# Kernel tuning notes

Measured on AMD Instinct MI355X. Metric: run time of the kernel, lower is better.

Reference implementation:

```python
import jax, jax.numpy as jnp
from jax import lax
import numpy as np

T, B, D, N = 1024, 32, 1024, 64
INIT_D_ALPHA, INIT_ALPHA_BIAS = 0.1, 2.0

def _xavier(key, n_out, n_in):
    lim = float(np.sqrt(6.0 / (n_in + n_out)))
    return jax.random.uniform(key, (n_out, n_in), jnp.float32, -lim, lim)

def setup_inputs() -> dict:
    key = jax.random.key(0)
    k = jax.random.split(key, 5)
    return {
        "x": jax.random.normal(k[0], (T, B, D), jnp.float32),
        "S0": jnp.zeros((B, N, N), jnp.float32),
        "W_k": _xavier(k[1], N, D),
        "W_v": _xavier(k[2], N, D),
        "W_q": _xavier(k[3], N, D),
        "W_alpha": _xavier(k[4], N, D),
        "d_alpha": jnp.full((N,), INIT_D_ALPHA, jnp.float32),
        "b_alpha": jnp.full((N,), INIT_ALPHA_BIAS, jnp.float32),
    }

def reference(x, S0, W_k, W_v, W_q, W_alpha, d_alpha, b_alpha):
    # Precompute all per-step projections as batched GEMMs: [T,B,N]
    k = jnp.einsum('tbd,nd->tbn', x, W_k)
    v = jnp.einsum('tbd,nd->tbn', x, W_v)
    q = jnp.einsum('tbd,nd->tbn', x, W_q)
    ax = jnp.einsum('tbd,nd->tbn', x, W_alpha)

    def step(S, inp):
        k_t, v_t, q_t, ax_t = inp  # each [B,N]
        retrieved = jnp.einsum('bij,bj->bi', S, k_t)            # S @ k
        alpha = jax.nn.sigmoid(ax_t + d_alpha * retrieved + b_alpha)  # [B,N]
        outer = v_t[:, :, None] * k_t[:, None, :]               # outer(v,k) [B,N,N]
        S = alpha[:, :, None] * S + (1.0 - alpha)[:, :, None] * outer
        h = jnp.einsum('bij,bj->bi', S, q_t)                    # S @ q
        out = h * jax.nn.silu(h)                                # self-gated
        return S, out

    S_final, output = lax.scan(step, S0, (k, v, q, ax))
    return output, S_final
```

## Files before the change

### kernel.cpp

```cpp
#include <hip/hip_runtime.h>
#include <math.h>

#define T_STEPS 1024
#define BATCH   32
#define DIM     1024
#define NST     64
#define TBN     ((size_t)T_STEPS * BATCH * NST)

typedef __attribute__((ext_vector_type(8))) short bf16x8;
typedef __attribute__((ext_vector_type(4))) float f32x4;

#define NLOG2E (-1.44269504088896340736f)

__device__ unsigned short g_khi[TBN];
__device__ unsigned short g_klo[TBN];
__device__ unsigned short g_qhi[TBN];
__device__ unsigned short g_qlo[TBN];

__device__ __forceinline__ void gload16(const void* g, void* l)
{
    __builtin_amdgcn_global_load_lds(
        (const __attribute__((address_space(1))) unsigned int*)g,
        (__attribute__((address_space(3))) unsigned int*)l, 16, 0, 0);
}

__device__ __forceinline__ void cvt8(float4 v0, float4 v1, bf16x8& hi, bf16x8& lo)
{
    float f[8] = {v0.x, v0.y, v0.z, v0.w, v1.x, v1.y, v1.z, v1.w};
    bf16x8 h, l;
    #pragma unroll
    for (int i = 0; i < 8; i++) {
        unsigned b = __float_as_uint(f[i]);
        h[i] = (short)(b >> 16);
        l[i] = (short)(__float_as_uint(f[i] - __uint_as_float(b & 0xffff0000u)) >> 16);
    }
    hi = h; lo = l;
}


__global__ __launch_bounds__(512, 1)
void proj_gemm_v2(const float* __restrict__ x,
                  const float* __restrict__ Wk,
                  const float* __restrict__ Wv,
                  const float* __restrict__ Wq,
                  const float* __restrict__ Wa,
                  const float* __restrict__ b_alpha,
                  float* __restrict__ ws)
{
    __shared__ float As[2][128][32];
    __shared__ float Bs[2][256][32];

    const int tid  = threadIdx.x;
    const int lane = tid & 63;
    const int w    = tid >> 6;
    const int m0   = blockIdx.x * 128;

    const int lrow  = lane >> 3;
    const int lgran = (lane & 7) ^ lrow;
    const float* ap0 = x + (size_t)(m0 + 16*w +     lrow) * DIM + lgran * 4;
    const float* ap1 = x + (size_t)(m0 + 16*w + 8 + lrow) * DIM + lgran * 4;
    const float* Wsrc = (w < 2) ? Wk : (w < 4) ? Wv : (w < 6) ? Wq : Wa;
    const float* bp0 = Wsrc + (size_t)((w & 1)*32 +  0 + lrow) * DIM + lgran * 4;
    const float* bp1 = Wsrc + (size_t)((w & 1)*32 +  8 + lrow) * DIM + lgran * 4;
    const float* bp2 = Wsrc + (size_t)((w & 1)*32 + 16 + lrow) * DIM + lgran * 4;
    const float* bp3 = Wsrc + (size_t)((w & 1)*32 + 24 + lrow) * DIM + lgran * 4;

    auto stage = [&](int kb, int buf) {
        const int ko = kb * 32;
        gload16(ap0 + ko, &As[buf][16*w     ][0]);
        gload16(ap1 + ko, &As[buf][16*w +  8][0]);
        gload16(bp0 + ko, &Bs[buf][32*w     ][0]);
        gload16(bp1 + ko, &Bs[buf][32*w +  8][0]);
        gload16(bp2 + ko, &Bs[buf][32*w + 16][0]);
        gload16(bp3 + ko, &Bs[buf][32*w + 24][0]);
    };

    const int fr = lane & 15;
    const int qi = lane >> 4;
    const int sx = fr & 7;
    const int mh = w >> 2;
    const int nq = w & 3;

    f32x4 acc[4][4];
    #pragma unroll
    for (int i = 0; i < 4; i++)
        #pragma unroll
        for (int j = 0; j < 4; j++)
            acc[i][j] = (f32x4)0.0f;

    stage(0, 0);
    __syncthreads();

    #pragma unroll 1
    for (int kb = 0; kb < 32; kb++) {
        const int buf = kb & 1;
        if (kb + 1 < 32) stage(kb + 1, buf ^ 1);

        bf16x8 ah[4], al[4], bh[4], bl[4];
        #pragma unroll
        for (int mt = 0; mt < 4; mt++) {
            const float* rp = &As[buf][mh*64 + mt*16 + fr][0];
            float4 v0 = *(const float4*)(rp + (((2*qi    ) ^ sx) * 4));
            float4 v1 = *(const float4*)(rp + (((2*qi + 1) ^ sx) * 4));
            cvt8(v0, v1, ah[mt], al[mt]);
        }
        #pragma unroll
        for (int nt = 0; nt < 4; nt++) {
            const float* rp = &Bs[buf][nq*64 + nt*16 + fr][0];
            float4 v0 = *(const float4*)(rp + (((2*qi    ) ^ sx) * 4));
            float4 v1 = *(const float4*)(rp + (((2*qi + 1) ^ sx) * 4));
            cvt8(v0, v1, bh[nt], bl[nt]);
        }
        #pragma unroll
        for (int mt = 0; mt < 4; mt++)
            #pragma unroll
            for (int nt = 0; nt < 4; nt++) {
                acc[mt][nt] = __builtin_amdgcn_mfma_f32_16x16x32_bf16(ah[mt], bh[nt], acc[mt][nt], 0, 0, 0);
                acc[mt][nt] = __builtin_amdgcn_mfma_f32_16x16x32_bf16(al[mt], bh[nt], acc[mt][nt], 0, 0, 0);
                acc[mt][nt] = __builtin_amdgcn_mfma_f32_16x16x32_bf16(ah[mt], bl[nt], acc[mt][nt], 0, 0, 0);
            }

        __syncthreads();
    }

    float* outb = ws + (size_t)nq * TBN;
    const int r0 = qi * 4;
    float bav[4];
    #pragma unroll
    for (int nt = 0; nt < 4; nt++)
        bav[nt] = (nq == 3) ? b_alpha[nt*16 + fr] : 0.0f;
    const float scl = (nq == 3) ? NLOG2E : 1.0f;
    #pragma unroll
    for (int mt = 0; mt < 4; mt++)
        #pragma unroll
        for (int nt = 0; nt < 4; nt++)
            #pragma unroll
            for (int r = 0; r < 4; r++) {
                const float val = (acc[mt][nt][r] + bav[nt]) * scl;
                const size_t idx = (size_t)(m0 + mh*64 + mt*16 + r0 + r) * NST + nt*16 + fr;
                if (nq != 2)
                    outb[idx] = val;
                if (nq == 0 || nq == 2) {
                    const unsigned bits = __float_as_uint(val);
                    const unsigned short hi = (unsigned short)(bits >> 16);
                    const float lof = val - __uint_as_float(bits & 0xffff0000u);
                    const unsigned short lo = (unsigned short)(__float_as_uint(lof) >> 16);
                    if (nq == 0) { g_khi[idx] = hi; g_klo[idx] = lo; }
                    else         { g_qhi[idx] = hi; g_qlo[idx] = lo; }
                }
            }
}


#define SCH 16
#define NCH (T_STEPS / SCH)

__global__ __launch_bounds__(256, 2)
void scan_gram2(const float* __restrict__ ws,
                const float* __restrict__ S0,
                const float* __restrict__ d_alpha,
                float* __restrict__ out)
{
    const float* kb_ = ws;
    const float* vb_ = ws + TBN;
    const float* ab_ = ws + 3 * TBN;

    __shared__ float k_st[2][SCH][64];
    __shared__ float va  [2][SCH][16];
    __shared__ float GG  [2][SCH][16][2];
    __shared__ unsigned short KH[2][SCH][64];
    __shared__ unsigned short KL[2][SCH][64];
    __shared__ unsigned short QH[2][SCH][64];
    __shared__ unsigned short QL[2][SCH][64];
    __shared__ float S_pvt[4][64];

    const int tid  = threadIdx.x;
    const int lane = tid & 63;
    const int w    = tid >> 6;
    const int bid  = blockIdx.x;
    const int b    = (bid & 7) * 4 + ((bid >> 3) & 3);
    const int rg   = bid >> 5;
    const int row  = rg * 4 + w;
    const int fr   = lane & 15;
    const int qi   = lane >> 4;

    const size_t stp = (size_t)BATCH * NST;

    float S = S0[((size_t)b * NST + row) * NST + lane];
    const float da_s = d_alpha[row] * NLOG2E;

    const float* ksrc = kb_ + (size_t)(4*w + qi) * stp + (size_t)b * NST + fr * 4;
    const float* vsrc = ((lane & 1) ? ab_ : vb_)
                      + (size_t)(lane >> 2) * stp + (size_t)b * NST + rg * 4;

    const unsigned short* pl_g = (w == 0) ? g_khi : (w == 1) ? g_klo
                               : (w == 2) ? g_qhi : g_qlo;
    const int prow  = lane >> 3;
    const int pgran = (lane & 7) ^ prow;
    const unsigned short* psrc0 = pl_g + ((size_t)prow       * stp + (size_t)b * NST + pgran * 8);
    const unsigned short* psrc1 = pl_g + ((size_t)(8 + prow) * stp + (size_t)b * NST + pgran * 8);

    auto stage = [&](int ch, int buf) {
        const size_t koff = (size_t)ch * SCH * stp;
        gload16(ksrc + koff, &k_st[buf][4*w][0]);
        if (w == 0)
            gload16(vsrc + koff, &va[buf][0][0]);
        unsigned short* pdst = (w == 0) ? &KH[buf][0][0] : (w == 1) ? &KL[buf][0][0]
                             : (w == 2) ? &QH[buf][0][0] : &QL[buf][0][0];
        gload16(psrc0 + koff, pdst);
        gload16(psrc1 + koff, pdst + 8 * 64);
    };

    const int c1 = (qi ^ (fr & 7)) * 8;
    const int c2 = c1 ^ 32;

    stage(0, 0);
    __syncthreads();

    float* op = out + (size_t)b * NST + row;
    float hv = 0.0f;

    #pragma unroll 1
    for (int ch = 0; ch < NCH; ch++) {
        const int buf = ch & 1;

        const bf16x8 Kh0 = *(const bf16x8*)&KH[buf][fr][c1];
        const bf16x8 Kh1 = *(const bf16x8*)&KH[buf][fr][c2];
        const bf16x8 Kl0 = *(const bf16x8*)&KL[buf][fr][c1];
        const bf16x8 Kl1 = *(const bf16x8*)&KL[buf][fr][c2];
        const bf16x8 Qh0 = *(const bf16x8*)&QH[buf][fr][c1];
        const bf16x8 Qh1 = *(const bf16x8*)&QH[buf][fr][c2];
        const bf16x8 Ql0 = *(const bf16x8*)&QL[buf][fr][c1];
        const bf16x8 Ql1 = *(const bf16x8*)&QL[buf][fr][c2];

        S_pvt[w][lane] = S;
        bf16x8 Sh0, Sl0, Sh1, Sl1;
        {
            float4 s0 = *(const float4*)&S_pvt[w][qi * 8];
            float4 s1 = *(const float4*)&S_pvt[w][qi * 8 + 4];
            cvt8(s0, s1, Sh0, Sl0);
            float4 s2 = *(const float4*)&S_pvt[w][32 + qi * 8];
            float4 s3 = *(const float4*)&S_pvt[w][32 + qi * 8 + 4];
            cvt8(s2, s3, Sh1, Sl1);
        }

        f32x4 aR0 = (f32x4)0.0f, aR1 = (f32x4)0.0f;
        f32x4 aH0 = (f32x4)0.0f, aH1 = (f32x4)0.0f;
        aR0 = __builtin_amdgcn_mfma_f32_16x16x32_bf16(Sh0, Kh0, aR0, 0, 0, 0);
        aR0 = __builtin_amdgcn_mfma_f32_16x16x32_bf16(Sh0, Kl0, aR0, 0, 0, 0);
        aR0 = __builtin_amdgcn_mfma_f32_16x16x32_bf16(Sl0, Kh0, aR0, 0, 0, 0);
        aR1 = __builtin_amdgcn_mfma_f32_16x16x32_bf16(Sh1, Kh1, aR1, 0, 0, 0);
        aR1 = __builtin_amdgcn_mfma_f32_16x16x32_bf16(Sh1, Kl1, aR1, 0, 0, 0);
        aR1 = __builtin_amdgcn_mfma_f32_16x16x32_bf16(Sl1, Kh1, aR1, 0, 0, 0);
        aH0 = __builtin_amdgcn_mfma_f32_16x16x32_bf16(Sh0, Qh0, aH0, 0, 0, 0);
        aH0 = __builtin_amdgcn_mfma_f32_16x16x32_bf16(Sh0, Ql0, aH0, 0, 0, 0);
        aH0 = __builtin_amdgcn_mfma_f32_16x16x32_bf16(Sl0, Qh0, aH0, 0, 0, 0);
        aH1 = __builtin_amdgcn_mfma_f32_16x16x32_bf16(Sh1, Qh1, aH1, 0, 0, 0);
        aH1 = __builtin_amdgcn_mfma_f32_16x16x32_bf16(Sh1, Ql1, aH1, 0, 0, 0);
        aH1 = __builtin_amdgcn_mfma_f32_16x16x32_bf16(Sl1, Qh1, aH1, 0, 0, 0);
        float R = aR0[0] + aR1[0];
        float H = aH0[0] + aH1[0];

        if (w == 0) {
            f32x4 aG = (f32x4)0.0f;
            aG = __builtin_amdgcn_mfma_f32_16x16x32_bf16(Kh0, Kh0, aG, 0, 0, 0);
            aG = __builtin_amdgcn_mfma_f32_16x16x32_bf16(Kh0, Kl0, aG, 0, 0, 0);
            aG = __builtin_amdgcn_mfma_f32_16x16x32_bf16(Kl0, Kh0, aG, 0, 0, 0);
            aG = __builtin_amdgcn_mfma_f32_16x16x32_bf16(Kh1, Kh1, aG, 0, 0, 0);
            aG = __builtin_amdgcn_mfma_f32_16x16x32_bf16(Kh1, Kl1, aG, 0, 0, 0);
            aG = __builtin_amdgcn_mfma_f32_16x16x32_bf16(Kl1, Kh1, aG, 0, 0, 0);
            #pragma unroll
            for (int r = 0; r < 4; r++) GG[buf][qi*4 + r][fr][0] = aG[r];
        } else if (w == 1) {
            f32x4 aQ = (f32x4)0.0f;
            aQ = __builtin_amdgcn_mfma_f32_16x16x32_bf16(Kh0, Qh0, aQ, 0, 0, 0);
            aQ = __builtin_amdgcn_mfma_f32_16x16x32_bf16(Kh0, Ql0, aQ, 0, 0, 0);
            aQ = __builtin_amdgcn_mfma_f32_16x16x32_bf16(Kl0, Qh0, aQ, 0, 0, 0);
            aQ = __builtin_amdgcn_mfma_f32_16x16x32_bf16(Kh1, Qh1, aQ, 0, 0, 0);
            aQ = __builtin_amdgcn_mfma_f32_16x16x32_bf16(Kh1, Ql1, aQ, 0, 0, 0);
            aQ = __builtin_amdgcn_mfma_f32_16x16x32_bf16(Kl1, Qh1, aQ, 0, 0, 0);
            #pragma unroll
            for (int r = 0; r < 4; r++) GG[buf][qi*4 + r][fr][1] = aQ[r];
        }

        __syncthreads();

        if (ch + 1 < NCH) stage(ch + 1, buf ^ 1);

        #pragma unroll
        for (int s = 0; s < SCH; s++) {
            const float  kcv = k_st[buf][s][lane];
            const float2 g2  = *(const float2*)&GG[buf][s][fr][0];
            const float  vv  = va[buf][s][w];
            const float  aa  = va[buf][s][4 + w];

            const float ret   = __int_as_float(
                __builtin_amdgcn_readlane(__float_as_int(R), s));
            const float z     = fmaf(da_s, ret, aa);
            const float e     = __builtin_amdgcn_exp2f(z);
            const float alpha = __builtin_amdgcn_rcpf(1.0f + e);
            const float bt    = (1.0f - alpha) * vv;

            R = fmaf(alpha, R, bt * g2.x);
            H = fmaf(alpha, H, bt * g2.y);
            S = fmaf(alpha, S, bt * kcv);

            hv = (lane == s) ? H : hv;
        }

        {
            const float sg = __builtin_amdgcn_rcpf(1.0f + __builtin_amdgcn_exp2f(hv * NLOG2E));
            const float o  = hv * hv * sg;
            if (lane < SCH)
                op[(size_t)(ch * SCH + lane) * stp] = o;
        }

        __syncthreads();
    }

    out[TBN + ((size_t)b * NST + row) * NST + lane] = S;
}


extern "C" void kernel_launch(void* const* d_in, const int* in_sizes, int n_in,
                              void* d_out, int out_size, void* d_ws, size_t ws_size,
                              hipStream_t stream)
{
    const float* x  = (const float*)d_in[0];
    const float* S0 = (const float*)d_in[1];
    const float* Wk = (const float*)d_in[2];
    const float* Wv = (const float*)d_in[3];
    const float* Wq = (const float*)d_in[4];
    const float* Wa = (const float*)d_in[5];
    const float* da = (const float*)d_in[6];
    const float* ba = (const float*)d_in[7];
    float* out = (float*)d_out;
    float* ws  = (float*)d_ws;

    proj_gemm_v2<<<dim3((T_STEPS * BATCH) / 128), 512, 0, stream>>>(x, Wk, Wv, Wq, Wa, ba, ws);

    scan_gram2<<<dim3(BATCH * 16), 256, 0, stream>>>(ws, S0, da, out);
}
```

Measured before the change: 382.2 us.

## Split projection GEMM across column halves and pipeline gram/retrieval in scan

The projection GEMM now runs two 256-thread blocks per 128-row tile, each covering two of the four projections, which doubles the grid and allows two blocks per CU. The scan kernel moves to triple-buffered staging and computes the K·K and K·Q gram for the next chunk ahead of time, so one barrier per chunk is removed. The inner recurrence is software-pipelined so the retrieved value for step s+1 comes from the previous R and gram value rather than waiting on the current update, shortening the serial dependency chain. The cost is more LDS, reloading x twice in the GEMM, and more complex register state in the scan loop.

```diff
diff --git a/kernel.cpp b/kernel.cpp
--- a/kernel.cpp
+++ b/kernel.cpp
@@ -11,6 +11,7 @@
 typedef __attribute__((ext_vector_type(4))) float f32x4;
 
 #define NLOG2E (-1.44269504088896340736f)
+#define MFMA16(a, b, c) __builtin_amdgcn_mfma_f32_16x16x32_bf16(a, b, c, 0, 0, 0)
 
 __device__ unsigned short g_khi[TBN];
 __device__ unsigned short g_klo[TBN];
@@ -38,8 +39,8 @@
 }
 
 
-__global__ __launch_bounds__(512, 1)
-void proj_gemm_v2(const float* __restrict__ x,
+__global__ __launch_bounds__(256, 2)
+void proj_gemm_v3(const float* __restrict__ x,
                   const float* __restrict__ Wk,
                   const float* __restrict__ Wv,
                   const float* __restrict__ Wq,
@@ -48,38 +49,41 @@
                   float* __restrict__ ws)
 {
     __shared__ float As[2][128][32];
-    __shared__ float Bs[2][256][32];
+    __shared__ float Bs[2][128][32];
 
     const int tid  = threadIdx.x;
     const int lane = tid & 63;
     const int w    = tid >> 6;
-    const int m0   = blockIdx.x * 128;
+    const int m0   = (blockIdx.x >> 1) * 128;
+    const int nh   = blockIdx.x & 1;
 
     const int lrow  = lane >> 3;
     const int lgran = (lane & 7) ^ lrow;
-    const float* ap0 = x + (size_t)(m0 + 16*w +     lrow) * DIM + lgran * 4;
-    const float* ap1 = x + (size_t)(m0 + 16*w + 8 + lrow) * DIM + lgran * 4;
-    const float* Wsrc = (w < 2) ? Wk : (w < 4) ? Wv : (w < 6) ? Wq : Wa;
-    const float* bp0 = Wsrc + (size_t)((w & 1)*32 +  0 + lrow) * DIM + lgran * 4;
-    const float* bp1 = Wsrc + (size_t)((w & 1)*32 +  8 + lrow) * DIM + lgran * 4;
-    const float* bp2 = Wsrc + (size_t)((w & 1)*32 + 16 + lrow) * DIM + lgran * 4;
-    const float* bp3 = Wsrc + (size_t)((w & 1)*32 + 24 + lrow) * DIM + lgran * 4;
+    const float* ap[4];
+    #pragma unroll
+    for (int i = 0; i < 4; i++)
+        ap[i] = x + (size_t)(m0 + 32*w + 8*i + lrow) * DIM + lgran * 4;
+    const int proj = nh * 2 + (w >> 1);
+    const float* Wsrc = (proj == 0) ? Wk : (proj == 1) ? Wv : (proj == 2) ? Wq : Wa;
+    const float* bp[4];
+    #pragma unroll
+    for (int i = 0; i < 4; i++)
+        bp[i] = Wsrc + (size_t)((w & 1)*32 + 8*i + lrow) * DIM + lgran * 4;
 
     auto stage = [&](int kb, int buf) {
         const int ko = kb * 32;
-        gload16(ap0 + ko, &As[buf][16*w     ][0]);
-        gload16(ap1 + ko, &As[buf][16*w +  8][0]);
-        gload16(bp0 + ko, &Bs[buf][32*w     ][0]);
-        gload16(bp1 + ko, &Bs[buf][32*w +  8][0]);
-        gload16(bp2 + ko, &Bs[buf][32*w + 16][0]);
-        gload16(bp3 + ko, &Bs[buf][32*w + 24][0]);
+        #pragma unroll
+        for (int i = 0; i < 4; i++) {
+            gload16(ap[i] + ko, &As[buf][32*w + 8*i][0]);
+            gload16(bp[i] + ko, &Bs[buf][32*w + 8*i][0]);
+        }
     };
 
     const int fr = lane & 15;
     const int qi = lane >> 4;
     const int sx = fr & 7;
-    const int mh = w >> 2;
-    const int nq = w & 3;
+    const int mh  = w >> 1;
+    const int nqh = w & 1;
 
     f32x4 acc[4][4];
     #pragma unroll
@@ -106,7 +110,7 @@
         }
         #pragma unroll
         for (int nt = 0; nt < 4; nt++) {
-            const float* rp = &Bs[buf][nq*64 + nt*16 + fr][0];
+            const float* rp = &Bs[buf][nqh*64 + nt*16 + fr][0];
             float4 v0 = *(const float4*)(rp + (((2*qi    ) ^ sx) * 4));
             float4 v1 = *(const float4*)(rp + (((2*qi + 1) ^ sx) * 4));
             cvt8(v0, v1, bh[nt], bl[nt]);
@@ -115,14 +119,15 @@
         for (int mt = 0; mt < 4; mt++)
             #pragma unroll
             for (int nt = 0; nt < 4; nt++) {
-                acc[mt][nt] = __builtin_amdgcn_mfma_f32_16x16x32_bf16(ah[mt], bh[nt], acc[mt][nt], 0, 0, 0);
-                acc[mt][nt] = __builtin_amdgcn_mfma_f32_16x16x32_bf16(al[mt], bh[nt], acc[mt][nt], 0, 0, 0);
-                acc[mt][nt] = __builtin_amdgcn_mfma_f32_16x16x32_bf16(ah[mt], bl[nt], acc[mt][nt], 0, 0, 0);
+                acc[mt][nt] = MFMA16(ah[mt], bh[nt], acc[mt][nt]);
+                acc[mt][nt] = MFMA16(al[mt], bh[nt], acc[mt][nt]);
+                acc[mt][nt] = MFMA16(ah[mt], bl[nt], acc[mt][nt]);
             }
 
         __syncthreads();
     }
 
+    const int nq = nh * 2 + nqh;
     float* outb = ws + (size_t)nq * TBN;
     const int r0 = qi * 4;
     float bav[4];
@@ -156,7 +161,7 @@
 #define NCH (T_STEPS / SCH)
 
 __global__ __launch_bounds__(256, 2)
-void scan_gram2(const float* __restrict__ ws,
+void scan_gram3(const float* __restrict__ ws,
                 const float* __restrict__ S0,
                 const float* __restrict__ d_alpha,
                 float* __restrict__ out)
@@ -165,13 +170,13 @@
     const float* vb_ = ws + TBN;
     const float* ab_ = ws + 3 * TBN;
 
-    __shared__ float k_st[2][SCH][64];
-    __shared__ float va  [2][SCH][16];
+    __shared__ float k_st[3][SCH][64];
+    __shared__ float va  [3][SCH][16];
     __shared__ float GG  [2][SCH][16][2];
-    __shared__ unsigned short KH[2][SCH][64];
-    __shared__ unsigned short KL[2][SCH][64];
-    __shared__ unsigned short QH[2][SCH][64];
-    __shared__ unsigned short QL[2][SCH][64];
+    __shared__ unsigned short KH[3][SCH][64];
+    __shared__ unsigned short KL[3][SCH][64];
+    __shared__ unsigned short QH[3][SCH][64];
+    __shared__ unsigned short QL[3][SCH][64];
     __shared__ float S_pvt[4][64];
 
     const int tid  = threadIdx.x;
@@ -214,24 +219,55 @@
     const int c1 = (qi ^ (fr & 7)) * 8;
     const int c2 = c1 ^ 32;
 
+    auto gram = [&](int fbs, int gdst) {
+        if (w == 0) {
+            const bf16x8 kh0 = *(const bf16x8*)&KH[fbs][fr][c1];
+            const bf16x8 kh1 = *(const bf16x8*)&KH[fbs][fr][c2];
+            const bf16x8 kl0 = *(const bf16x8*)&KL[fbs][fr][c1];
+            const bf16x8 kl1 = *(const bf16x8*)&KL[fbs][fr][c2];
+            f32x4 aG = (f32x4)0.0f;
+            aG = MFMA16(kh0, kh0, aG); aG = MFMA16(kh0, kl0, aG); aG = MFMA16(kl0, kh0, aG);
+            aG = MFMA16(kh1, kh1, aG); aG = MFMA16(kh1, kl1, aG); aG = MFMA16(kl1, kh1, aG);
+            #pragma unroll
+            for (int r = 0; r < 4; r++) GG[gdst][qi*4 + r][fr][0] = aG[r];
+        } else if (w == 1) {
+            const bf16x8 kh0 = *(const bf16x8*)&KH[fbs][fr][c1];
+            const bf16x8 kh1 = *(const bf16x8*)&KH[fbs][fr][c2];
+            const bf16x8 kl0 = *(const bf16x8*)&KL[fbs][fr][c1];
+            const bf16x8 kl1 = *(const bf16x8*)&KL[fbs][fr][c2];
+            const bf16x8 qh0 = *(const bf16x8*)&QH[fbs][fr][c1];
+            const bf16x8 qh1 = *(const bf16x8*)&QH[fbs][fr][c2];
+            const bf16x8 ql0 = *(const bf16x8*)&QL[fbs][fr][c1];
+            const bf16x8 ql1 = *(const bf16x8*)&QL[fbs][fr][c2];
+            f32x4 aQ = (f32x4)0.0f;
+            aQ = MFMA16(kh0, qh0, aQ); aQ = MFMA16(kh0, ql0, aQ); aQ = MFMA16(kl0, qh0, aQ);
+            aQ = MFMA16(kh1, qh1, aQ); aQ = MFMA16(kh1, ql1, aQ); aQ = MFMA16(kl1, qh1, aQ);
+            #pragma unroll
+            for (int r = 0; r < 4; r++) GG[gdst][qi*4 + r][fr][1] = aQ[r];
+        }
+    };
+
     stage(0, 0);
+    stage(1, 1);
     __syncthreads();
+    gram(0, 0);
+    __syncthreads();
 
     float* op = out + (size_t)b * NST + row;
-    float hv = 0.0f;
 
     #pragma unroll 1
     for (int ch = 0; ch < NCH; ch++) {
-        const int buf = ch & 1;
-
-        const bf16x8 Kh0 = *(const bf16x8*)&KH[buf][fr][c1];
-        const bf16x8 Kh1 = *(const bf16x8*)&KH[buf][fr][c2];
-        const bf16x8 Kl0 = *(const bf16x8*)&KL[buf][fr][c1];
-        const bf16x8 Kl1 = *(const bf16x8*)&KL[buf][fr][c2];
-        const bf16x8 Qh0 = *(const bf16x8*)&QH[buf][fr][c1];
-        const bf16x8 Qh1 = *(const bf16x8*)&QH[buf][fr][c2];
-        const bf16x8 Ql0 = *(const bf16x8*)&QL[buf][fr][c1];
-        const bf16x8 Ql1 = *(const bf16x8*)&QL[buf][fr][c2];
+        const int fb = ch % 3;
+        const int gb = ch & 1;
+
+        const bf16x8 Kh0 = *(const bf16x8*)&KH[fb][fr][c1];
+        const bf16x8 Kh1 = *(const bf16x8*)&KH[fb][fr][c2];
+        const bf16x8 Kl0 = *(const bf16x8*)&KL[fb][fr][c1];
+        const bf16x8 Kl1 = *(const bf16x8*)&KL[fb][fr][c2];
+        const bf16x8 Qh0 = *(const bf16x8*)&QH[fb][fr][c1];
+        const bf16x8 Qh1 = *(const bf16x8*)&QH[fb][fr][c2];
+        const bf16x8 Ql0 = *(const bf16x8*)&QL[fb][fr][c1];
+        const bf16x8 Ql1 = *(const bf16x8*)&QL[fb][fr][c2];
 
         S_pvt[w][lane] = S;
         bf16x8 Sh0, Sl0, Sh1, Sl1;
@@ -246,66 +282,57 @@
 
         f32x4 aR0 = (f32x4)0.0f, aR1 = (f32x4)0.0f;
         f32x4 aH0 = (f32x4)0.0f, aH1 = (f32x4)0.0f;
-        aR0 = __builtin_amdgcn_mfma_f32_16x16x32_bf16(Sh0, Kh0, aR0, 0, 0, 0);
-        aR0 = __builtin_amdgcn_mfma_f32_16x16x32_bf16(Sh0, Kl0, aR0, 0, 0, 0);
-        aR0 = __builtin_amdgcn_mfma_f32_16x16x32_bf16(Sl0, Kh0, aR0, 0, 0, 0);
-        aR1 = __builtin_amdgcn_mfma_f32_16x16x32_bf16(Sh1, Kh1, aR1, 0, 0, 0);
-        aR1 = __builtin_amdgcn_mfma_f32_16x16x32_bf16(Sh1, Kl1, aR1, 0, 0, 0);
-        aR1 = __builtin_amdgcn_mfma_f32_16x16x32_bf16(Sl1, Kh1, aR1, 0, 0, 0);
-        aH0 = __builtin_amdgcn_mfma_f32_16x16x32_bf16(Sh0, Qh0, aH0, 0, 0, 0);
-        aH0 = __builtin_amdgcn_mfma_f32_16x16x32_bf16(Sh0, Ql0, aH0, 0, 0, 0);
-        aH0 = __builtin_amdgcn_mfma_f32_16x16x32_bf16(Sl0, Qh0, aH0, 0, 0, 0);
-        aH1 = __builtin_amdgcn_mfma_f32_16x16x32_bf16(Sh1, Qh1, aH1, 0, 0, 0);
-        aH1 = __builtin_amdgcn_mfma_f32_16x16x32_bf16(Sh1, Ql1, aH1, 0, 0, 0);
-        aH1 = __builtin_amdgcn_mfma_f32_16x16x32_bf16(Sl1, Qh1, aH1, 0, 0, 0);
+        aR0 = MFMA16(Sh0, Kh0, aR0); aR0 = MFMA16(Sh0, Kl0, aR0); aR0 = MFMA16(Sl0, Kh0, aR0);
+        aR1 = MFMA16(Sh1, Kh1, aR1); aR1 = MFMA16(Sh1, Kl1, aR1); aR1 = MFMA16(Sl1, Kh1, aR1);
+        aH0 = MFMA16(Sh0, Qh0, aH0); aH0 = MFMA16(Sh0, Ql0, aH0); aH0 = MFMA16(Sl0, Qh0, aH0);
+        aH1 = MFMA16(Sh1, Qh1, aH1); aH1 = MFMA16(Sh1, Ql1, aH1); aH1 = MFMA16(Sl1, Qh1, aH1);
         float R = aR0[0] + aR1[0];
         float H = aH0[0] + aH1[0];
 
-        if (w == 0) {
-            f32x4 aG = (f32x4)0.0f;
-            aG = __builtin_amdgcn_mfma_f32_16x16x32_bf16(Kh0, Kh0, aG, 0, 0, 0);
-            aG = __builtin_amdgcn_mfma_f32_16x16x32_bf16(Kh0, Kl0, aG, 0, 0, 0);
-            aG = __builtin_amdgcn_mfma_f32_16x16x32_bf16(Kl0, Kh0, aG, 0, 0, 0);
-            aG = __builtin_amdgcn_mfma_f32_16x16x32_bf16(Kh1, Kh1, aG, 0, 0, 0);
-            aG = __builtin_amdgcn_mfma_f32_16x16x32_bf16(Kh1, Kl1, aG, 0, 0, 0);
-            aG = __builtin_amdgcn_mfma_f32_16x16x32_bf16(Kl1, Kh1, aG, 0, 0, 0);
-            #pragma unroll
-            for (int r = 0; r < 4; r++) GG[buf][qi*4 + r][fr][0] = aG[r];
-        } else if (w == 1) {
-            f32x4 aQ = (f32x4)0.0f;
-            aQ = __builtin_amdgcn_mfma_f32_16x16x32_bf16(Kh0, Qh0, aQ, 0, 0, 0);
-            aQ = __builtin_amdgcn_mfma_f32_16x16x32_bf16(Kh0, Ql0, aQ, 0, 0, 0);
-            aQ = __builtin_amdgcn_mfma_f32_16x16x32_bf16(Kl0, Qh0, aQ, 0, 0, 0);
-            aQ = __builtin_amdgcn_mfma_f32_16x16x32_bf16(Kh1, Qh1, aQ, 0, 0, 0);
-            aQ = __builtin_amdgcn_mfma_f32_16x16x32_bf16(Kh1, Ql1, aQ, 0, 0, 0);
-            aQ = __builtin_amdgcn_mfma_f32_16x16x32_bf16(Kl1, Qh1, aQ, 0, 0, 0);
-            #pragma unroll
-            for (int r = 0; r < 4; r++) GG[buf][qi*4 + r][fr][1] = aQ[r];
-        }
-
-        __syncthreads();
-
-        if (ch + 1 < NCH) stage(ch + 1, buf ^ 1);
+        if (ch + 1 < NCH) gram((ch + 1) % 3, gb ^ 1);
+
+        if (ch + 2 < NCH) stage(ch + 2, (ch + 2) % 3);
+
+        float alpha_p = 1.0f, vv_p = 0.0f;
+        float g_p = 0.0f, gq_p = 0.0f, kc_p = 0.0f;
+        float vvG  = 0.0f;
+        float diff = __int_as_float(__builtin_amdgcn_readlane(__float_as_int(R), 0));
+        float hv   = 0.0f;
 
         #pragma unroll
         for (int s = 0; s < SCH; s++) {
-            const float  kcv = k_st[buf][s][lane];
-            const float2 g2  = *(const float2*)&GG[buf][s][fr][0];
-            const float  vv  = va[buf][s][w];
-            const float  aa  = va[buf][s][4 + w];
-
-            const float ret   = __int_as_float(
-                __builtin_amdgcn_readlane(__float_as_int(R), s));
+            const float2 g2  = *(const float2*)&GG[gb][s][fr][0];
+            const float  kcv = k_st[fb][s][lane];
+            const float  vv  = va[fb][s][w];
+            const float  aa  = va[fb][s][4 + w];
+
+            const float bt_p = (1.0f - alpha_p) * vv_p;
+            R = fmaf(alpha_p, R, bt_p * g_p);
+            H = fmaf(alpha_p, H, bt_p * gq_p);
+            S = fmaf(alpha_p, S, bt_p * kc_p);
+            if (s >= 1) hv = (lane == s - 1) ? H : hv;
+
+            const float rlR = __int_as_float(__builtin_amdgcn_readlane(__float_as_int(R), s + 1));
+            const float rlG = __int_as_float(__builtin_amdgcn_readlane(__float_as_int(g2.x), s + 1));
+
+            const float ret   = fmaf(alpha_p, diff, vvG);
             const float z     = fmaf(da_s, ret, aa);
             const float e     = __builtin_amdgcn_exp2f(z);
             const float alpha = __builtin_amdgcn_rcpf(1.0f + e);
-            const float bt    = (1.0f - alpha) * vv;
-
-            R = fmaf(alpha, R, bt * g2.x);
-            H = fmaf(alpha, H, bt * g2.y);
-            S = fmaf(alpha, S, bt * kcv);
-
-            hv = (lane == s) ? H : hv;
+
+            const float vvG_n  = vv * rlG;
+            const float diff_n = rlR - vvG_n;
+
+            alpha_p = alpha; vv_p = vv;
+            g_p = g2.x; gq_p = g2.y; kc_p = kcv;
+            vvG = vvG_n; diff = diff_n;
+        }
+
+        {
+            const float bt_p = (1.0f - alpha_p) * vv_p;
+            H = fmaf(alpha_p, H, bt_p * gq_p);
+            S = fmaf(alpha_p, S, bt_p * kc_p);
+            hv = (lane == SCH - 1) ? H : hv;
         }
 
         {
@@ -337,7 +364,7 @@
     float* out = (float*)d_out;
     float* ws  = (float*)d_ws;
 
-    proj_gemm_v2<<<dim3((T_STEPS * BATCH) / 128), 512, 0, stream>>>(x, Wk, Wv, Wq, Wa, ba, ws);
-
-    scan_gram2<<<dim3(BATCH * 16), 256, 0, stream>>>(ws, S0, da, out);
-}
+    proj_gemm_v3<<<dim3((T_STEPS * BATCH) / 128 * 2), 256, 0, stream>>>(x, Wk, Wv, Wq, Wa, ba, ws);
+
+    scan_gram3<<<dim3(BATCH * 16), 256, 0, stream>>>(ws, S0, da, out);
+}
```

Result: faster. 367.3 us (-3.9%).

## Split projection GEMM across two blocks per row tile and use RNE bf16 splitting

Applied to the files above, without the earlier changes.

The projection GEMM now launches twice as many 256-thread blocks. Each block computes half of the four projections (two of k/v/q/alpha) for a 128-row tile, which halves shared memory for B and allows two blocks per CU. The x tile is loaded redundantly by both blocks. The bf16 hi/lo split also changes from truncation to round-to-nearest-even via HIP bf16 intrinsics, which improves precision but may cost more ALU work in the conversion hot loop, and it also affects the scan kernel's cvt8.

```diff
diff --git a/kernel.cpp b/kernel.cpp
--- a/kernel.cpp
+++ b/kernel.cpp
@@ -1,4 +1,5 @@
 #include <hip/hip_runtime.h>
+#include <hip/hip_bf16.h>
 #include <math.h>
 
 #define T_STEPS 1024
@@ -11,6 +12,7 @@
 typedef __attribute__((ext_vector_type(4))) float f32x4;
 
 #define NLOG2E (-1.44269504088896340736f)
+#define MFMA16(a, b, c) __builtin_amdgcn_mfma_f32_16x16x32_bf16(a, b, c, 0, 0, 0)
 
 __device__ unsigned short g_khi[TBN];
 __device__ unsigned short g_klo[TBN];
@@ -24,22 +26,32 @@
         (__attribute__((address_space(3))) unsigned int*)l, 16, 0, 0);
 }
 
+__device__ __forceinline__ void split1_rne(float v, unsigned short& hi, unsigned short& lo)
+{
+    __hip_bfloat16 hb = __float2bfloat16(v);
+    unsigned short hraw; __builtin_memcpy(&hraw, &hb, 2);
+    float hf = __bfloat162float(hb);
+    __hip_bfloat16 lb = __float2bfloat16(v - hf);
+    unsigned short lraw; __builtin_memcpy(&lraw, &lb, 2);
+    hi = hraw; lo = lraw;
+}
+
 __device__ __forceinline__ void cvt8(float4 v0, float4 v1, bf16x8& hi, bf16x8& lo)
 {
     float f[8] = {v0.x, v0.y, v0.z, v0.w, v1.x, v1.y, v1.z, v1.w};
     bf16x8 h, l;
     #pragma unroll
     for (int i = 0; i < 8; i++) {
-        unsigned b = __float_as_uint(f[i]);
-        h[i] = (short)(b >> 16);
-        l[i] = (short)(__float_as_uint(f[i] - __uint_as_float(b & 0xffff0000u)) >> 16);
+        unsigned short hr, lr;
+        split1_rne(f[i], hr, lr);
+        h[i] = (short)hr; l[i] = (short)lr;
     }
     hi = h; lo = l;
 }
 
 
-__global__ __launch_bounds__(512, 1)
-void proj_gemm_v2(const float* __restrict__ x,
+__global__ __launch_bounds__(256, 2)
+void proj_gemm_v3(const float* __restrict__ x,
                   const float* __restrict__ Wk,
                   const float* __restrict__ Wv,
                   const float* __restrict__ Wq,
@@ -48,38 +60,41 @@
                   float* __restrict__ ws)
 {
     __shared__ float As[2][128][32];
-    __shared__ float Bs[2][256][32];
+    __shared__ float Bs[2][128][32];
 
     const int tid  = threadIdx.x;
     const int lane = tid & 63;
     const int w    = tid >> 6;
-    const int m0   = blockIdx.x * 128;
+    const int m0   = (blockIdx.x >> 1) * 128;
+    const int nh   = blockIdx.x & 1;
 
     const int lrow  = lane >> 3;
     const int lgran = (lane & 7) ^ lrow;
-    const float* ap0 = x + (size_t)(m0 + 16*w +     lrow) * DIM + lgran * 4;
-    const float* ap1 = x + (size_t)(m0 + 16*w + 8 + lrow) * DIM + lgran * 4;
-    const float* Wsrc = (w < 2) ? Wk : (w < 4) ? Wv : (w < 6) ? Wq : Wa;
-    const float* bp0 = Wsrc + (size_t)((w & 1)*32 +  0 + lrow) * DIM + lgran * 4;
-    const float* bp1 = Wsrc + (size_t)((w & 1)*32 +  8 + lrow) * DIM + lgran * 4;
-    const float* bp2 = Wsrc + (size_t)((w & 1)*32 + 16 + lrow) * DIM + lgran * 4;
-    const float* bp3 = Wsrc + (size_t)((w & 1)*32 + 24 + lrow) * DIM + lgran * 4;
+    const float* ap[4];
+    #pragma unroll
+    for (int i = 0; i < 4; i++)
+        ap[i] = x + (size_t)(m0 + 32*w + 8*i + lrow) * DIM + lgran * 4;
+    const int proj = nh * 2 + (w >> 1);
+    const float* Wsrc = (proj == 0) ? Wk : (proj == 1) ? Wv : (proj == 2) ? Wq : Wa;
+    const float* bp[4];
+    #pragma unroll
+    for (int i = 0; i < 4; i++)
+        bp[i] = Wsrc + (size_t)((w & 1)*32 + 8*i + lrow) * DIM + lgran * 4;
 
     auto stage = [&](int kb, int buf) {
         const int ko = kb * 32;
-        gload16(ap0 + ko, &As[buf][16*w     ][0]);
-        gload16(ap1 + ko, &As[buf][16*w +  8][0]);
-        gload16(bp0 + ko, &Bs[buf][32*w     ][0]);
-        gload16(bp1 + ko, &Bs[buf][32*w +  8][0]);
-        gload16(bp2 + ko, &Bs[buf][32*w + 16][0]);
-        gload16(bp3 + ko, &Bs[buf][32*w + 24][0]);
+        #pragma unroll
+        for (int i = 0; i < 4; i++) {
+            gload16(ap[i] + ko, &As[buf][32*w + 8*i][0]);
+            gload16(bp[i] + ko, &Bs[buf][32*w + 8*i][0]);
+        }
     };
 
     const int fr = lane & 15;
     const int qi = lane >> 4;
     const int sx = fr & 7;
-    const int mh = w >> 2;
-    const int nq = w & 3;
+    const int mh  = w >> 1;
+    const int nqh = w & 1;
 
     f32x4 acc[4][4];
     #pragma unroll
@@ -106,7 +121,7 @@
         }
         #pragma unroll
         for (int nt = 0; nt < 4; nt++) {
-            const float* rp = &Bs[buf][nq*64 + nt*16 + fr][0];
+            const float* rp = &Bs[buf][nqh*64 + nt*16 + fr][0];
             float4 v0 = *(const float4*)(rp + (((2*qi    ) ^ sx) * 4));
             float4 v1 = *(const float4*)(rp + (((2*qi + 1) ^ sx) * 4));
             cvt8(v0, v1, bh[nt], bl[nt]);
@@ -115,14 +130,15 @@
         for (int mt = 0; mt < 4; mt++)
             #pragma unroll
             for (int nt = 0; nt < 4; nt++) {
-                acc[mt][nt] = __builtin_amdgcn_mfma_f32_16x16x32_bf16(ah[mt], bh[nt], acc[mt][nt], 0, 0, 0);
-                acc[mt][nt] = __builtin_amdgcn_mfma_f32_16x16x32_bf16(al[mt], bh[nt], acc[mt][nt], 0, 0, 0);
-                acc[mt][nt] = __builtin_amdgcn_mfma_f32_16x16x32_bf16(ah[mt], bl[nt], acc[mt][nt], 0, 0, 0);
+                acc[mt][nt] = MFMA16(ah[mt], bh[nt], acc[mt][nt]);
+                acc[mt][nt] = MFMA16(al[mt], bh[nt], acc[mt][nt]);
+                acc[mt][nt] = MFMA16(ah[mt], bl[nt], acc[mt][nt]);
             }
 
         __syncthreads();
     }
 
+    const int nq = nh * 2 + nqh;
     float* outb = ws + (size_t)nq * TBN;
     const int r0 = qi * 4;
     float bav[4];
@@ -141,12 +157,10 @@
                 if (nq != 2)
                     outb[idx] = val;
                 if (nq == 0 || nq == 2) {
-                    const unsigned bits = __float_as_uint(val);
-                    const unsigned short hi = (unsigned short)(bits >> 16);
-                    const float lof = val - __uint_as_float(bits & 0xffff0000u);
-                    const unsigned short lo = (unsigned short)(__float_as_uint(lof) >> 16);
-                    if (nq == 0) { g_khi[idx] = hi; g_klo[idx] = lo; }
-                    else         { g_qhi[idx] = hi; g_qlo[idx] = lo; }
+                    unsigned short hr, lr;
+                    split1_rne(val, hr, lr);
+                    if (nq == 0) { g_khi[idx] = hr; g_klo[idx] = lr; }
+                    else         { g_qhi[idx] = hr; g_qlo[idx] = lr; }
                 }
             }
 }
@@ -246,39 +260,23 @@
 
         f32x4 aR0 = (f32x4)0.0f, aR1 = (f32x4)0.0f;
         f32x4 aH0 = (f32x4)0.0f, aH1 = (f32x4)0.0f;
-        aR0 = __builtin_amdgcn_mfma_f32_16x16x32_bf16(Sh0, Kh0, aR0, 0, 0, 0);
-        aR0 = __builtin_amdgcn_mfma_f32_16x16x32_bf16(Sh0, Kl0, aR0, 0, 0, 0);
-        aR0 = __builtin_amdgcn_mfma_f32_16x16x32_bf16(Sl0, Kh0, aR0, 0, 0, 0);
-        aR1 = __builtin_amdgcn_mfma_f32_16x16x32_bf16(Sh1, Kh1, aR1, 0, 0, 0);
-        aR1 = __builtin_amdgcn_mfma_f32_16x16x32_bf16(Sh1, Kl1, aR1, 0, 0, 0);
-        aR1 = __builtin_amdgcn_mfma_f32_16x16x32_bf16(Sl1, Kh1, aR1, 0, 0, 0);
-        aH0 = __builtin_amdgcn_mfma_f32_16x16x32_bf16(Sh0, Qh0, aH0, 0, 0, 0);
-        aH0 = __builtin_amdgcn_mfma_f32_16x16x32_bf16(Sh0, Ql0, aH0, 0, 0, 0);
-        aH0 = __builtin_amdgcn_mfma_f32_16x16x32_bf16(Sl0, Qh0, aH0, 0, 0, 0);
-        aH1 = __builtin_amdgcn_mfma_f32_16x16x32_bf16(Sh1, Qh1, aH1, 0, 0, 0);
-        aH1 = __builtin_amdgcn_mfma_f32_16x16x32_bf16(Sh1, Ql1, aH1, 0, 0, 0);
-        aH1 = __builtin_amdgcn_mfma_f32_16x16x32_bf16(Sl1, Qh1, aH1, 0, 0, 0);
+        aR0 = MFMA16(Sh0, Kh0, aR0); aR0 = MFMA16(Sh0, Kl0, aR0); aR0 = MFMA16(Sl0, Kh0, aR0);
+        aR1 = MFMA16(Sh1, Kh1, aR1); aR1 = MFMA16(Sh1, Kl1, aR1); aR1 = MFMA16(Sl1, Kh1, aR1);
+        aH0 = MFMA16(Sh0, Qh0, aH0); aH0 = MFMA16(Sh0, Ql0, aH0); aH0 = MFMA16(Sl0, Qh0, aH0);
+        aH1 = MFMA16(Sh1, Qh1, aH1); aH1 = MFMA16(Sh1, Ql1, aH1); aH1 = MFMA16(Sl1, Qh1, aH1);
         float R = aR0[0] + aR1[0];
         float H = aH0[0] + aH1[0];
 
         if (w == 0) {
             f32x4 aG = (f32x4)0.0f;
-            aG = __builtin_amdgcn_mfma_f32_16x16x32_bf16(Kh0, Kh0, aG, 0, 0, 0);
-            aG = __builtin_amdgcn_mfma_f32_16x16x32_bf16(Kh0, Kl0, aG, 0, 0, 0);
-            aG = __builtin_amdgcn_mfma_f32_16x16x32_bf16(Kl0, Kh0, aG, 0, 0, 0);
-            aG = __builtin_amdgcn_mfma_f32_16x16x32_bf16(Kh1, Kh1, aG, 0, 0, 0);
-            aG = __builtin_amdgcn_mfma_f32_16x16x32_bf16(Kh1, Kl1, aG, 0, 0, 0);
-            aG = __builtin_amdgcn_mfma_f32_16x16x32_bf16(Kl1, Kh1, aG, 0, 0, 0);
+            aG = MFMA16(Kh0, Kh0, aG); aG = MFMA16(Kh0, Kl0, aG); aG = MFMA16(Kl0, Kh0, aG);
+            aG = MFMA16(Kh1, Kh1, aG); aG = MFMA16(Kh1, Kl1, aG); aG = MFMA16(Kl1, Kh1, aG);
             #pragma unroll
             for (int r = 0; r < 4; r++) GG[buf][qi*4 + r][fr][0] = aG[r];
         } else if (w == 1) {
             f32x4 aQ = (f32x4)0.0f;
-            aQ = __builtin_amdgcn_mfma_f32_16x16x32_bf16(Kh0, Qh0, aQ, 0, 0, 0);
-            aQ = __builtin_amdgcn_mfma_f32_16x16x32_bf16(Kh0, Ql0, aQ, 0, 0, 0);
-            aQ = __builtin_amdgcn_mfma_f32_16x16x32_bf16(Kl0, Qh0, aQ, 0, 0, 0);
-            aQ = __builtin_amdgcn_mfma_f32_16x16x32_bf16(Kh1, Qh1, aQ, 0, 0, 0);
-            aQ = __builtin_amdgcn_mfma_f32_16x16x32_bf16(Kh1, Ql1, aQ, 0, 0, 0);
-            aQ = __builtin_amdgcn_mfma_f32_16x16x32_bf16(Kl1, Qh1, aQ, 0, 0, 0);
+            aQ = MFMA16(Kh0, Qh0, aQ); aQ = MFMA16(Kh0, Ql0, aQ); aQ = MFMA16(Kl0, Qh0, aQ);
+            aQ = MFMA16(Kh1, Qh1, aQ); aQ = MFMA16(Kh1, Ql1, aQ); aQ = MFMA16(Kl1, Qh1, aQ);
             #pragma unroll
             for (int r = 0; r < 4; r++) GG[buf][qi*4 + r][fr][1] = aQ[r];
         }
@@ -337,7 +335,7 @@
     float* out = (float*)d_out;
     float* ws  = (float*)d_ws;
 
-    proj_gemm_v2<<<dim3((T_STEPS * BATCH) / 128), 512, 0, stream>>>(x, Wk, Wv, Wq, Wa, ba, ws);
+    proj_gemm_v3<<<dim3((T_STEPS * BATCH) / 128 * 2), 256, 0, stream>>>(x, Wk, Wv, Wq, Wa, ba, ws);
 
     scan_gram2<<<dim3(BATCH * 16), 256, 0, stream>>>(ws, S0, da, out);
 }
```

Result: faster. 356.2 us (-6.8%).
